# Performance work log

Measured on AMD Instinct MI355X. Metric: run time of the kernel, lower is better.

Reference implementation:

```python
import jax, jax.numpy as jnp
import numpy as np

B, D_IN, H1, D_OUT = 32768, 256, 256, 64
E, T, MU = 32, 16, 0.01


def setup_inputs() -> dict:
    key = jax.random.key(0)
    ks = jax.random.split(key, 9)
    s = lambda *sh: 1.0 / np.sqrt(sh[-2])  # not used; torch default init approximated below
    return {
        "backbone_output": jax.random.normal(ks[0], (B, D_IN), dtype=jnp.float32),
        "task": jax.random.randint(ks[1], (B,), 0, T),
        # expert MLP params, stacked across experts (weights stored [E, in, out])
        "W1": jax.random.normal(ks[2], (E, D_IN, H1), dtype=jnp.float32) * (1.0 / np.sqrt(D_IN)),
        "b1": jnp.zeros((E, H1), dtype=jnp.float32),
        "W2": jax.random.normal(ks[3], (E, H1, D_OUT), dtype=jnp.float32) * (1.0 / np.sqrt(H1)),
        "b2": jnp.zeros((E, D_OUT), dtype=jnp.float32),
        # attention params (torch.randn init)
        "task_queries": jax.random.normal(ks[4], (T, D_OUT), dtype=jnp.float32),
        "key_matricies": jax.random.normal(ks[5], (E, D_OUT, D_OUT), dtype=jnp.float32),
        "value_matricies": jax.random.normal(ks[6], (E, D_OUT, D_OUT), dtype=jnp.float32),
    }


def reference(backbone_output, task, W1, b1, W2, b2, task_queries, key_matricies, value_matricies):
    # all experts run densely on the full batch
    h = jax.nn.relu(jnp.einsum('bi,eih->beh', backbone_output, W1) + b1)      # [B,E,H1]
    expert_outputs = jnp.einsum('beh,eho->beo', h, W2) + b2                   # [B,E,D_OUT]
    # per-expert key/value projections
    expert_keys = jnp.einsum('bei,eij->bej', expert_outputs, key_matricies)    # [B,E,D_OUT]
    expert_values = jnp.einsum('bei,eij->bej', expert_outputs, value_matricies)
    # attention over experts using the per-task query
    q = task_queries[task]                                                     # [B,D_OUT]
    attention_scores = jnp.einsum('bej,bj->be', expert_keys, q)                # [B,E]
    attention_weights = jax.nn.softmax(attention_scores, axis=-1)
    tower_input = jnp.einsum('be,bej->bj', attention_weights, expert_values)   # [B,D_OUT]
    eps = jnp.float32(1e-6)
    reg_loss_term = -(1.0 / E) * MU * jnp.sum(attention_weights + eps)
    return tower_input, reg_loss_term
```

## Files before the change

kernel.cpp:

```cpp
#include <hip/hip_runtime.h>
#include <hip/hip_fp16.h>

#define NTHR 512
#define BM   128
#define NBLK 256
#define NEXP 32

using f16x8 = __attribute__((ext_vector_type(8))) _Float16;
using f16x4 = __attribute__((ext_vector_type(4))) _Float16;
using f32x4 = __attribute__((ext_vector_type(4))) float;
using u32x4 = __attribute__((ext_vector_type(4))) unsigned int;
using u32x2 = __attribute__((ext_vector_type(2))) unsigned int;

static constexpr size_t ESTRIDE_B = 182272;

__device__ __forceinline__ unsigned short f2h(float x){
  _Float16 h = (_Float16)x; return __builtin_bit_cast(unsigned short, h);
}

typedef __attribute__((address_space(3))) void lds_void;
typedef const __attribute__((address_space(1))) void glb_void;
__device__ __forceinline__ void gll16(const void* g, void* l){
  __builtin_amdgcn_global_load_lds((glb_void*)g, (lds_void*)l, 16, 0, 0);
}

#define VMW(N)  asm volatile("s_waitcnt vmcnt(" #N ")" ::: "memory")
#define LGKM0   asm volatile("s_waitcnt lgkmcnt(0)" ::: "memory")
#define SB      __builtin_amdgcn_sched_barrier(0)
#define BARRIER do { SB; __builtin_amdgcn_s_barrier(); SB; } while(0)

__global__ __launch_bounds__(256) void prep_w1frag(const float* __restrict__ W1,
                                                   unsigned short* __restrict__ strm){
  const int e = blockIdx.x >> 3, kc = blockIdx.x & 7;
  const float* se = W1 + (size_t)e*65536 + (size_t)kc*32*256;
  unsigned short* de = strm + (size_t)e*91136 + kc*8192;
  for (int fl = threadIdx.x; fl < 1024; fl += 256){
    const int ct = fl >> 6, l = fl & 63;
    const float* s0 = se + (size_t)((l>>4)*8)*256 + ct*16 + (l&15);
    union { unsigned short s[8]; u32x4 v; } h8;
    #pragma unroll
    for (int j = 0; j < 8; j++) h8.s[j] = f2h(s0[(size_t)j*256]);
    *reinterpret_cast<u32x4*>(&de[fl*8]) = h8.v;
  }
}

__global__ __launch_bounds__(256) void prep_wvp(
    const float* __restrict__ W2, const float* __restrict__ V,
    const float* __restrict__ Km, const float* __restrict__ Q,
    const float* __restrict__ b1, const float* __restrict__ b2,
    unsigned short* __restrict__ strm, float* __restrict__ out)
{
  const int e = blockIdx.x >> 3, oct = blockIdx.x & 7;
  const int t = threadIdx.x;
  __shared__ float lv[64*64];
  __shared__ float ktlT[64*16];
  __shared__ float lw2[32*64];

  for (int i = t; i < 1024; i += 256)
    *reinterpret_cast<float4*>(&lv[i*4]) = *reinterpret_cast<const float4*>(V + (size_t)e*4096 + i*4);
  for (int i = t; i < 512; i += 256)
    *reinterpret_cast<float4*>(&lw2[i*4]) = *reinterpret_cast<const float4*>(W2 + (size_t)e*16384 + (size_t)oct*2048 + i*4);
  #pragma unroll
  for (int pass = 0; pass < 4; pass++){
    const int id = t + pass*256;
    const int tt = id >> 6, i = id & 63;
    const float4* Kr = reinterpret_cast<const float4*>(Km + (size_t)(e*64 + i)*64);
    const float4* qr = reinterpret_cast<const float4*>(Q + tt*64);
    float s = 0.f;
    #pragma unroll
    for (int j = 0; j < 16; j++){ float4 a = Kr[j], b = qr[j]; s += a.x*b.x+a.y*b.y+a.z*b.z+a.w*b.w; }
    ktlT[i*16 + tt] = s;
  }
  __syncthreads();

  const int k2 = oct*32 + (t >> 3);
  const int cb = t & 7;
  const int c0 = cb*12;
  const float* w2r = &lw2[(t>>3)*64];
  const float* gp[3]; int gs[3]; bool gv[3];
  #pragma unroll
  for (int q = 0; q < 3; q++){
    const int cg = c0 + q*4;
    gv[q] = (cg < 80);
    if (cg < 64){ gp[q] = &lv[cg];        gs[q] = 64; }
    else        { gp[q] = &ktlT[cg - 64]; gs[q] = 16; }
  }
  float pv[12];
  #pragma unroll
  for (int n = 0; n < 12; n++) pv[n] = 0.f;
  for (int i = 0; i < 64; i++){
    const float w = w2r[i];
    #pragma unroll
    for (int q = 0; q < 3; q++){
      if (gv[q]){
        const float4 vq = *reinterpret_cast<const float4*>(gp[q] + i*gs[q]);
        pv[q*4+0] += w*vq.x; pv[q*4+1] += w*vq.y; pv[q*4+2] += w*vq.z; pv[q*4+3] += w*vq.w;
      }
    }
  }
  const int wn_ = k2 >> 7, fn = (k2 >> 4) & 7, fnp = fn >> 1, half = fn & 1;
  const int g2 = (k2 >> 2) & 3, jj = k2 & 3;
  unsigned short* fb = strm + (size_t)e*91136 + (wn_ ? 77824 : 65536);
  #pragma unroll
  for (int n = 0; n < 12; n++){
    const int cc = c0 + n;
    if (cc < 64){
      const int ct = cc >> 4, lc = cc & 15, l = g2*16 + lc;
      fb[(fnp*6+ct)*512 + l*8 + half*4 + jj] = f2h(pv[n]);
    } else if (cc < 80){
      const int lc = cc - 64, l = g2*16 + lc;
      const float s = pv[n];
      const unsigned short hi = f2h(s);
      const float rem = s - (float)__builtin_bit_cast(_Float16, hi);
      fb[(fnp*6+4)*512 + l*8 + half*4 + jj] = hi;
      fb[(fnp*6+5)*512 + l*8 + half*4 + jj] = f2h(rem);
    }
  }
  if (oct == 0){
    float* b1d = reinterpret_cast<float*>((char*)strm + (size_t)e*ESTRIDE_B + 180224);
    b1d[t] = b1[e*256 + t];
  }
  if (oct == 1 && t < 80){
    float s = 0.f;
    if (t < 64){ for (int i = 0; i < 64; i++) s += b2[e*64+i]*lv[i*64+t]; }
    else       { for (int i = 0; i < 64; i++) s += b2[e*64+i]*ktlT[i*16 + (t-64)]; }
    float* bd = reinterpret_cast<float*>((char*)strm + (size_t)e*ESTRIDE_B + 181248);
    bd[t] = s;
  }
  if (blockIdx.x == 0 && t == 0) out[2097152] = -10.24032768f;
}

__global__ __launch_bounds__(NTHR, 2) __attribute__((amdgpu_waves_per_eu(2, 2)))
void moe_main(const float* __restrict__ X, const int* __restrict__ task,
              const unsigned short* __restrict__ strm, float* __restrict__ out)
{
  __shared__ unsigned short smem[75776];
  unsigned char* exch = (unsigned char*)smem + 98304;

  const int tid  = threadIdx.x;
  const int lane = tid & 63;
  const int wid  = tid >> 6;
  const int g    = lane >> 4;
  const int c    = lane & 15;
  const int wm   = wid >> 1, wn = wid & 1;
  const int row0 = blockIdx.x * BM;

  auto issue48 = [&](const unsigned short* src, int sloth){
    #pragma unroll
    for (int q = 0; q < 6; q++)
      gll16(src + q*4096 + tid*8, &smem[sloth + q*4096 + tid*8]);
  };
  auto issue32 = [&](const unsigned short* src, int sloth){
    #pragma unroll
    for (int q = 0; q < 4; q++)
      gll16(src + q*4096 + tid*8, &smem[sloth + q*4096 + tid*8]);
  };
  auto issueAux = [&](const unsigned short* es_, int k){
    gll16(es_ + 90112 + lane*8, &smem[73728 + k*1024 + lane*8]);
    gll16(es_ + 90624 + lane*8, &smem[73728 + k*1024 + 512 + lane*8]);
  };

  f16x8 af[2][8];
  #pragma unroll
  for (int fm = 0; fm < 2; fm++){
    const float* xr = X + (size_t)(row0 + wm*32 + fm*16 + c)*256;
    #pragma unroll
    for (int kc = 0; kc < 8; kc++){
      const f32x4 v0 = *reinterpret_cast<const f32x4*>(xr + kc*32 + g*8);
      const f32x4 v1 = *reinterpret_cast<const f32x4*>(xr + kc*32 + g*8 + 4);
      union { unsigned short s[8]; f16x8 h; } h8;
      #pragma unroll
      for (int j = 0; j < 4; j++){ h8.s[j] = f2h(v0[j]); h8.s[4+j] = f2h(v1[j]); }
      af[fm][kc] = h8.h;
    }
  }
  const int4 tq = *reinterpret_cast<const int4*>(&task[row0 + wm*32 + wn*16 + g*4]);
  const int tsk4[4] = {tq.x, tq.y, tq.z, tq.w};

  VMW(0);

  issue48(strm,          0);
  issue48(strm + 24576,  24576);
  issueAux(strm, 0);

  f32x4 oacc[4];
  float m_[4], d_[4];
  #pragma unroll
  for (int j = 0; j < 4; j++){
    m_[j] = -1e30f; d_[j] = 0.f;
    #pragma unroll
    for (int ct = 0; ct < 4; ct++) oacc[ct][j] = 0.f;
  }

#define G1STEP(BASEH, KC) do { \
    f16x8 bfr_[8]; \
    _Pragma("unroll") \
    for (int fnl = 0; fnl < 8; fnl++) \
      bfr_[fnl] = *reinterpret_cast<const f16x8*>(&smem[(BASEH) + (wn*8+fnl)*512 + lane*8]); \
    _Pragma("unroll") \
    for (int fnl = 0; fnl < 8; fnl++){ \
      acc1[fnl][0] = __builtin_amdgcn_mfma_f32_16x16x32_f16(bfr_[fnl], af[0][KC], acc1[fnl][0], 0,0,0); \
      acc1[fnl][1] = __builtin_amdgcn_mfma_f32_16x16x32_f16(bfr_[fnl], af[1][KC], acc1[fnl][1], 0,0,0); \
    } \
  } while(0)

#define MSTEP(FNP) do { \
    u32x4 pr[6]; \
    _Pragma("unroll") \
    for (int i = 0; i < 6; i++) \
      pr[i] = *reinterpret_cast<const u32x4*>(&smem[49152 + wn*12288 + ((FNP)*6+i)*512 + lane*8]); \
    const f32x4 b1a = *reinterpret_cast<const f32x4*>(b1f + wn*128 + (2*(FNP)+0)*16 + g*4); \
    const f32x4 b1b = *reinterpret_cast<const f32x4*>(b1f + wn*128 + (2*(FNP)+1)*16 + g*4); \
    _Pragma("unroll") \
    for (int half = 0; half < 2; half++){ \
      const int fnl = (FNP)*2 + half; \
      const f32x4 bb = half ? b1b : b1a; \
      f16x4 a0, a1; \
      _Pragma("unroll") \
      for (int j = 0; j < 4; j++){ \
        a0[j] = (_Float16)fmaxf(acc1[fnl][0][j] + bb[j], 0.f); \
        a1[j] = (_Float16)fmaxf(acc1[fnl][1][j] + bb[j], 0.f); \
      } \
      _Pragma("unroll") \
      for (int ct = 0; ct < 6; ct++){ \
        union { u32x4 v; struct { f16x4 lo, hi; } h; } u; u.v = pr[ct]; \
        const f16x4 bfr = half ? u.h.hi : u.h.lo; \
        const int ci = (ct < 5) ? ct : 4; \
        p0[ci] = __builtin_amdgcn_mfma_f32_16x16x16f16(a0, bfr, p0[ci], 0,0,0); \
        p1[ci] = __builtin_amdgcn_mfma_f32_16x16x16f16(a1, bfr, p1[ci], 0,0,0); \
      } \
    } \
  } while(0)

#define XW(ACC, EB) do { \
    _Pragma("unroll") \
    for (int ct = 0; ct < 4; ct++){ \
      union { unsigned short s[4]; u32x2 v; } p_; \
      _Pragma("unroll") \
      for (int j = 0; j < 4; j++) p_.s[j] = f2h(ACC[ct][j]); \
      *reinterpret_cast<u32x2*>((EB) + ct*512 + lane*8) = p_.v; \
    } \
    *reinterpret_cast<f32x4*>((EB) + 2048 + lane*16) = ACC[4]; \
  } while(0)

#define XFIN(B2F) do { \
    const unsigned char* ebS = exch + (wm*2 + wn)*6144 + wn*3072; \
    const unsigned char* ebP = exch + (wm*2 + (wn^1))*6144 + wn*3072; \
    float b2c[4]; \
    _Pragma("unroll") \
    for (int ct = 0; ct < 4; ct++) b2c[ct] = (B2F)[ct*16 + c]; \
    const float b2s = (B2F)[64 + c]; \
    f32x4 pvv[4]; \
    _Pragma("unroll") \
    for (int ct = 0; ct < 4; ct++){ \
      union { u32x2 v; unsigned short s[4]; } pa_, pb_; \
      pa_.v = *reinterpret_cast<const u32x2*>(ebS + ct*512 + lane*8); \
      pb_.v = *reinterpret_cast<const u32x2*>(ebP + ct*512 + lane*8); \
      _Pragma("unroll") \
      for (int j = 0; j < 4; j++) \
        pvv[ct][j] = (float)__builtin_bit_cast(_Float16, pa_.s[j]) \
                   + (float)__builtin_bit_cast(_Float16, pb_.s[j]) + b2c[ct]; \
    } \
    const f32x4 s1 = *reinterpret_cast<const f32x4*>(ebS + 2048 + lane*16); \
    const f32x4 s2 = *reinterpret_cast<const f32x4*>(ebP + 2048 + lane*16); \
    _Pragma("unroll") \
    for (int j = 0; j < 4; j++){ \
      const float sv = s1[j] + s2[j] + b2s; \
      const float s  = __shfl(sv, (lane & 48) | tsk4[j]); \
      const float mn = fmaxf(m_[j], s); \
      const float al = __expf(m_[j] - mn); \
      const float p  = __expf(s - mn); \
      d_[j] = d_[j]*al + p; \
      m_[j] = mn; \
      _Pragma("unroll") \
      for (int ct = 0; ct < 4; ct++) \
        oacc[ct][j] = oacc[ct][j]*al + p*pvv[ct][j]; \
    } \
  } while(0)

  for (int e = 0; e < NEXP; e++){
    const unsigned short* es  = strm + (size_t)e*91136;
    const unsigned short* esn = (e == NEXP-1) ? strm : es + 91136;
    const int pA = (e & 1) * 24576;
    const int pB = 24576 - pA;
    const float* b1f = reinterpret_cast<const float*>(&smem[73728 + (e & 1)*1024]);
    f32x4 acc1[8][2] = {};

    VMW(8); BARRIER;
    G1STEP(pA,          0);
    if (e > 0){
      const float* b2p = reinterpret_cast<const float*>(&smem[73728 + ((e+1) & 1)*1024]) + 256;
      XFIN(b2p);
    }
    G1STEP(pA +  8192,  1);
    G1STEP(pA + 16384,  2);

    VMW(2); BARRIER;
    issue32(es + 49152, pA);
    issue48(es + 65536, 49152);
    G1STEP(pB,          3);
    G1STEP(pB +  8192,  4);
    G1STEP(pB + 16384,  5);

    VMW(6); BARRIER;
    issue48(esn, pB);
    G1STEP(pA,          6);
    G1STEP(pA +  8192,  7);

    VMW(6); BARRIER;
    issue48(esn + 24576, pA);
    f32x4 p0[5] = {}, p1[5] = {};
    MSTEP(0); MSTEP(1); MSTEP(2); MSTEP(3);

    BARRIER;
    {
      unsigned char* eb = exch + wid*6144;
      XW(p0, eb);
      XW(p1, eb + 3072);
    }
    issueAux(esn, (e+1) & 1);
    LGKM0;
  }

  BARRIER;
  {
    const float* b2p = reinterpret_cast<const float*>(&smem[73728 + (31 & 1)*1024]) + 256;
    XFIN(b2p);
  }
#undef XFIN
#undef XW
#undef MSTEP
#undef G1STEP

  #pragma unroll
  for (int j = 0; j < 4; j++){
    const float inv = 1.f / d_[j];
    float* orow = out + (size_t)(row0 + wm*32 + wn*16 + g*4 + j)*64;
    #pragma unroll
    for (int ct = 0; ct < 4; ct++)
      orow[ct*16 + c] = oacc[ct][j]*inv;
  }
}

extern "C" void kernel_launch(void* const* d_in, const int* in_sizes, int n_in,
                              void* d_out, int out_size, void* d_ws, size_t ws_size,
                              hipStream_t hs)
{
  (void)in_sizes; (void)n_in; (void)out_size; (void)ws_size;
  const float* X   = (const float*)d_in[0];
  const int*   tsk = (const int*)  d_in[1];
  const float* W1  = (const float*)d_in[2];
  const float* b1  = (const float*)d_in[3];
  const float* W2  = (const float*)d_in[4];
  const float* b2  = (const float*)d_in[5];
  const float* Q   = (const float*)d_in[6];
  const float* Km  = (const float*)d_in[7];
  const float* Vm  = (const float*)d_in[8];
  float* out = (float*)d_out;

  unsigned short* strm = (unsigned short*)d_ws;

  prep_w1frag<<<dim3(256), dim3(256), 0, hs>>>(W1, strm);
  prep_wvp  <<<dim3(256), dim3(256), 0, hs>>>(W2, Vm, Km, Q, b1, b2, strm, out);
  moe_main  <<<dim3(NBLK), dim3(NTHR), 0, hs>>>(X, tsk, strm, out);
}
```

Measured before the change: 242.9 us.

## Halve block to 4 waves, stage X in LDS, stream W1 in small double-buffered chunks

The main kernel moves from 8 waves to 4 waves per block. Each wave now computes 64 rows instead of 32, so it keeps 8x4 MFMA accumulators. The fp16-converted X tile is stored in shared memory and A fragments are reloaded per K-step, replacing the register-resident copy. W1 is streamed in 16 KB chunks through two LDS slots, with one barrier per K-step, and the second-GEMM partial exchange between wave pairs is reorganised to match. The aim is to raise MFMA work per B-fragment load and change the latency and occupancy balance. The cost is more LDS reads for A, more barriers, higher register pressure, and fewer waves available to hide latency.

```diff
diff --git a/kernel.cpp b/kernel.cpp
--- a/kernel.cpp
+++ b/kernel.cpp
@@ -1,7 +1,7 @@
 #include <hip/hip_runtime.h>
 #include <hip/hip_fp16.h>
 
-#define NTHR 512
+#define NTHR 256
 #define BM   128
 #define NBLK 256
 #define NEXP 32
@@ -130,7 +130,7 @@
   if (blockIdx.x == 0 && t == 0) out[2097152] = -10.24032768f;
 }
 
-__global__ __launch_bounds__(NTHR, 2) __attribute__((amdgpu_waves_per_eu(2, 2)))
+__global__ __launch_bounds__(NTHR, 1)
 void moe_main(const float* __restrict__ X, const int* __restrict__ task,
               const unsigned short* __restrict__ strm, float* __restrict__ out)
 {
@@ -145,63 +145,73 @@
   const int wm   = wid >> 1, wn = wid & 1;
   const int row0 = blockIdx.x * BM;
 
-  auto issue48 = [&](const unsigned short* src, int sloth){
+  auto issue16 = [&](const unsigned short* src, int sloth){
+    #pragma unroll
+    for (int q = 0; q < 4; q++)
+      gll16(src + q*2048 + tid*8, &smem[sloth + q*2048 + tid*8]);
+  };
+  auto issueM = [&](const unsigned short* es_, int half){
     #pragma unroll
     for (int q = 0; q < 6; q++)
-      gll16(src + q*4096 + tid*8, &smem[sloth + q*4096 + tid*8]);
-  };
-  auto issue32 = [&](const unsigned short* src, int sloth){
-    #pragma unroll
-    for (int q = 0; q < 4; q++)
-      gll16(src + q*4096 + tid*8, &smem[sloth + q*4096 + tid*8]);
+      gll16(es_ + 65536 + half*12288 + q*2048 + tid*8,
+            &smem[49152 + half*12288 + q*2048 + tid*8]);
   };
   auto issueAux = [&](const unsigned short* es_, int k){
     gll16(es_ + 90112 + lane*8, &smem[73728 + k*1024 + lane*8]);
     gll16(es_ + 90624 + lane*8, &smem[73728 + k*1024 + 512 + lane*8]);
   };
 
-  f16x8 af[2][8];
-  #pragma unroll
-  for (int fm = 0; fm < 2; fm++){
-    const float* xr = X + (size_t)(row0 + wm*32 + fm*16 + c)*256;
-    #pragma unroll
-    for (int kc = 0; kc < 8; kc++){
-      const f32x4 v0 = *reinterpret_cast<const f32x4*>(xr + kc*32 + g*8);
-      const f32x4 v1 = *reinterpret_cast<const f32x4*>(xr + kc*32 + g*8 + 4);
-      union { unsigned short s[8]; f16x8 h; } h8;
+  #pragma unroll
+  for (int p = 0; p < 16; p++){
+    const int id  = p*256 + tid;
+    const int row = id >> 5, k0 = (id & 31)*8;
+    const float4 v0 = *reinterpret_cast<const float4*>(X + (size_t)(row0+row)*256 + k0);
+    const float4 v1 = *reinterpret_cast<const float4*>(X + (size_t)(row0+row)*256 + k0 + 4);
+    union { unsigned short s[8]; u32x4 v; } h8;
+    h8.s[0]=f2h(v0.x); h8.s[1]=f2h(v0.y); h8.s[2]=f2h(v0.z); h8.s[3]=f2h(v0.w);
+    h8.s[4]=f2h(v1.x); h8.s[5]=f2h(v1.y); h8.s[6]=f2h(v1.z); h8.s[7]=f2h(v1.w);
+    const int l = (row & 15) | (((k0 >> 3) & 3) << 4);
+    *reinterpret_cast<u32x4*>(&smem[((row>>4)*8 + (k0>>5))*512 + l*8]) = h8.v;
+  }
+
+  int tsk[2][4];
+  {
+    const int4 qa = *reinterpret_cast<const int4*>(&task[row0 + wm*64 + (wn*2+0)*16 + g*4]);
+    const int4 qb = *reinterpret_cast<const int4*>(&task[row0 + wm*64 + (wn*2+1)*16 + g*4]);
+    tsk[0][0]=qa.x; tsk[0][1]=qa.y; tsk[0][2]=qa.z; tsk[0][3]=qa.w;
+    tsk[1][0]=qb.x; tsk[1][1]=qb.y; tsk[1][2]=qb.z; tsk[1][3]=qb.w;
+  }
+
+  issueAux(strm, 0);
+  issue16(strm,         32768);
+  issue16(strm +  8192, 40960);
+  LGKM0;
+
+  f32x4 oacc[2][4];
+  float m_[2][4], d_[2][4];
+  #pragma unroll
+  for (int o = 0; o < 2; o++)
+    #pragma unroll
+    for (int j = 0; j < 4; j++){
+      m_[o][j] = -1e30f; d_[o][j] = 0.f;
       #pragma unroll
-      for (int j = 0; j < 4; j++){ h8.s[j] = f2h(v0[j]); h8.s[4+j] = f2h(v1[j]); }
-      af[fm][kc] = h8.h;
-    }
-  }
-  const int4 tq = *reinterpret_cast<const int4*>(&task[row0 + wm*32 + wn*16 + g*4]);
-  const int tsk4[4] = {tq.x, tq.y, tq.z, tq.w};
-
-  VMW(0);
-
-  issue48(strm,          0);
-  issue48(strm + 24576,  24576);
-  issueAux(strm, 0);
-
-  f32x4 oacc[4];
-  float m_[4], d_[4];
-  #pragma unroll
-  for (int j = 0; j < 4; j++){
-    m_[j] = -1e30f; d_[j] = 0.f;
-    #pragma unroll
-    for (int ct = 0; ct < 4; ct++) oacc[ct][j] = 0.f;
-  }
-
-#define G1STEP(BASEH, KC) do { \
-    f16x8 bfr_[8]; \
+      for (int ct = 0; ct < 4; ct++) oacc[o][ct][j] = 0.f;
+    }
+  f32x4 p[4][5];
+
+#define G1STEP(SLOTH, KC) do { \
+    f16x8 bf_[8], ab_[4]; \
     _Pragma("unroll") \
     for (int fnl = 0; fnl < 8; fnl++) \
-      bfr_[fnl] = *reinterpret_cast<const f16x8*>(&smem[(BASEH) + (wn*8+fnl)*512 + lane*8]); \
-    _Pragma("unroll") \
-    for (int fnl = 0; fnl < 8; fnl++){ \
-      acc1[fnl][0] = __builtin_amdgcn_mfma_f32_16x16x32_f16(bfr_[fnl], af[0][KC], acc1[fnl][0], 0,0,0); \
-      acc1[fnl][1] = __builtin_amdgcn_mfma_f32_16x16x32_f16(bfr_[fnl], af[1][KC], acc1[fnl][1], 0,0,0); \
-    } \
+      bf_[fnl] = *reinterpret_cast<const f16x8*>(&smem[(SLOTH) + (wn*8+fnl)*512 + lane*8]); \
+    _Pragma("unroll") \
+    for (int fmi = 0; fmi < 4; fmi++) \
+      ab_[fmi] = *reinterpret_cast<const f16x8*>(&smem[((wm*4+fmi)*8 + (KC))*512 + lane*8]); \
+    _Pragma("unroll") \
+    for (int fnl = 0; fnl < 8; fnl++) \
+      _Pragma("unroll") \
+      for (int fmi = 0; fmi < 4; fmi++) \
+        acc1[fnl][fmi] = __builtin_amdgcn_mfma_f32_16x16x32_f16(bf_[fnl], ab_[fmi], acc1[fnl][fmi], 0,0,0); \
   } while(0)
 
 #define MSTEP(FNP) do { \
@@ -215,130 +225,128 @@
     for (int half = 0; half < 2; half++){ \
       const int fnl = (FNP)*2 + half; \
       const f32x4 bb = half ? b1b : b1a; \
-      f16x4 a0, a1; \
+      f16x4 a0, a1, a2, a3; \
       _Pragma("unroll") \
       for (int j = 0; j < 4; j++){ \
         a0[j] = (_Float16)fmaxf(acc1[fnl][0][j] + bb[j], 0.f); \
         a1[j] = (_Float16)fmaxf(acc1[fnl][1][j] + bb[j], 0.f); \
+        a2[j] = (_Float16)fmaxf(acc1[fnl][2][j] + bb[j], 0.f); \
+        a3[j] = (_Float16)fmaxf(acc1[fnl][3][j] + bb[j], 0.f); \
       } \
       _Pragma("unroll") \
       for (int ct = 0; ct < 6; ct++){ \
         union { u32x4 v; struct { f16x4 lo, hi; } h; } u; u.v = pr[ct]; \
         const f16x4 bfr = half ? u.h.hi : u.h.lo; \
         const int ci = (ct < 5) ? ct : 4; \
-        p0[ci] = __builtin_amdgcn_mfma_f32_16x16x16f16(a0, bfr, p0[ci], 0,0,0); \
-        p1[ci] = __builtin_amdgcn_mfma_f32_16x16x16f16(a1, bfr, p1[ci], 0,0,0); \
+        p[0][ci] = __builtin_amdgcn_mfma_f32_16x16x16f16(a0, bfr, p[0][ci], 0,0,0); \
+        p[1][ci] = __builtin_amdgcn_mfma_f32_16x16x16f16(a1, bfr, p[1][ci], 0,0,0); \
+        p[2][ci] = __builtin_amdgcn_mfma_f32_16x16x16f16(a2, bfr, p[2][ci], 0,0,0); \
+        p[3][ci] = __builtin_amdgcn_mfma_f32_16x16x16f16(a3, bfr, p[3][ci], 0,0,0); \
       } \
-    } \
-  } while(0)
-
-#define XW(ACC, EB) do { \
+    } } while(0)
+
+#define XW1(ACC, SLOT) do { \
+    unsigned char* eb_ = exch + (SLOT)*3072; \
     _Pragma("unroll") \
     for (int ct = 0; ct < 4; ct++){ \
       union { unsigned short s[4]; u32x2 v; } p_; \
       _Pragma("unroll") \
       for (int j = 0; j < 4; j++) p_.s[j] = f2h(ACC[ct][j]); \
-      *reinterpret_cast<u32x2*>((EB) + ct*512 + lane*8) = p_.v; \
+      *reinterpret_cast<u32x2*>(eb_ + ct*512 + lane*8) = p_.v; \
     } \
-    *reinterpret_cast<f32x4*>((EB) + 2048 + lane*16) = ACC[4]; \
+    *reinterpret_cast<f32x4*>(eb_ + 2048 + lane*16) = ACC[4]; \
   } while(0)
 
-#define XFIN(B2F) do { \
-    const unsigned char* ebS = exch + (wm*2 + wn)*6144 + wn*3072; \
-    const unsigned char* ebP = exch + (wm*2 + (wn^1))*6144 + wn*3072; \
+#define XFIN1(ACC, SLOT, OI) do { \
+    const unsigned char* eb_ = exch + (SLOT)*3072; \
+    f32x4 pvv[4]; \
+    _Pragma("unroll") \
+    for (int ct = 0; ct < 4; ct++){ \
+      union { u32x2 v; unsigned short s[4]; } pb_; \
+      pb_.v = *reinterpret_cast<const u32x2*>(eb_ + ct*512 + lane*8); \
+      _Pragma("unroll") \
+      for (int j = 0; j < 4; j++) \
+        pvv[ct][j] = ACC[ct][j] + (float)__builtin_bit_cast(_Float16, pb_.s[j]) + b2c[ct]; \
+    } \
+    const f32x4 s2 = *reinterpret_cast<const f32x4*>(eb_ + 2048 + lane*16); \
+    _Pragma("unroll") \
+    for (int j = 0; j < 4; j++){ \
+      const float sv = ACC[4][j] + s2[j] + b2s; \
+      const float s  = __shfl(sv, (lane & 48) | tsk[OI][j]); \
+      const float mn = fmaxf(m_[OI][j], s); \
+      const float al = __expf(m_[OI][j] - mn); \
+      const float pe = __expf(s - mn); \
+      d_[OI][j] = d_[OI][j]*al + pe; \
+      m_[OI][j] = mn; \
+      _Pragma("unroll") \
+      for (int ct = 0; ct < 4; ct++) \
+        oacc[OI][ct][j] = oacc[OI][ct][j]*al + pe*pvv[ct][j]; \
+    } } while(0)
+
+#define XFINALL(B2F) do { \
     float b2c[4]; \
     _Pragma("unroll") \
     for (int ct = 0; ct < 4; ct++) b2c[ct] = (B2F)[ct*16 + c]; \
     const float b2s = (B2F)[64 + c]; \
-    f32x4 pvv[4]; \
-    _Pragma("unroll") \
-    for (int ct = 0; ct < 4; ct++){ \
-      union { u32x2 v; unsigned short s[4]; } pa_, pb_; \
-      pa_.v = *reinterpret_cast<const u32x2*>(ebS + ct*512 + lane*8); \
-      pb_.v = *reinterpret_cast<const u32x2*>(ebP + ct*512 + lane*8); \
-      _Pragma("unroll") \
-      for (int j = 0; j < 4; j++) \
-        pvv[ct][j] = (float)__builtin_bit_cast(_Float16, pa_.s[j]) \
-                   + (float)__builtin_bit_cast(_Float16, pb_.s[j]) + b2c[ct]; \
-    } \
-    const f32x4 s1 = *reinterpret_cast<const f32x4*>(ebS + 2048 + lane*16); \
-    const f32x4 s2 = *reinterpret_cast<const f32x4*>(ebP + 2048 + lane*16); \
-    _Pragma("unroll") \
-    for (int j = 0; j < 4; j++){ \
-      const float sv = s1[j] + s2[j] + b2s; \
-      const float s  = __shfl(sv, (lane & 48) | tsk4[j]); \
-      const float mn = fmaxf(m_[j], s); \
-      const float al = __expf(m_[j] - mn); \
-      const float p  = __expf(s - mn); \
-      d_[j] = d_[j]*al + p; \
-      m_[j] = mn; \
-      _Pragma("unroll") \
-      for (int ct = 0; ct < 4; ct++) \
-        oacc[ct][j] = oacc[ct][j]*al + p*pvv[ct][j]; \
-    } \
+    if (wn == 0){ XFIN1(p[0], wm*4+0, 0); XFIN1(p[1], wm*4+1, 1); } \
+    else        { XFIN1(p[2], wm*4+2, 0); XFIN1(p[3], wm*4+3, 1); } \
   } while(0)
 
   for (int e = 0; e < NEXP; e++){
     const unsigned short* es  = strm + (size_t)e*91136;
     const unsigned short* esn = (e == NEXP-1) ? strm : es + 91136;
-    const int pA = (e & 1) * 24576;
-    const int pB = 24576 - pA;
     const float* b1f = reinterpret_cast<const float*>(&smem[73728 + (e & 1)*1024]);
-    f32x4 acc1[8][2] = {};
-
-    VMW(8); BARRIER;
-    G1STEP(pA,          0);
+    f32x4 acc1[8][4] = {};
+
+    VMW(4); BARRIER;
+    G1STEP(32768, 0);
     if (e > 0){
       const float* b2p = reinterpret_cast<const float*>(&smem[73728 + ((e+1) & 1)*1024]) + 256;
-      XFIN(b2p);
-    }
-    G1STEP(pA +  8192,  1);
-    G1STEP(pA + 16384,  2);
-
-    VMW(2); BARRIER;
-    issue32(es + 49152, pA);
-    issue48(es + 65536, 49152);
-    G1STEP(pB,          3);
-    G1STEP(pB +  8192,  4);
-    G1STEP(pB + 16384,  5);
+      XFINALL(b2p);
+    }
+    VMW(0); BARRIER; issue16(es + 2*8192, 32768);                    G1STEP(40960, 1);
+    VMW(0); BARRIER; issue16(es + 3*8192, 40960);                    G1STEP(32768, 2);
+    VMW(0); BARRIER; issue16(es + 4*8192, 32768);                    G1STEP(40960, 3);
+    VMW(0); BARRIER; issue16(es + 5*8192, 40960); issueM(es, 0);     G1STEP(32768, 4);
+    VMW(6); BARRIER; issue16(es + 6*8192, 32768); issueM(es, 1);     G1STEP(40960, 5);
+    VMW(6); BARRIER; issue16(es + 7*8192, 40960); issueAux(esn, (e+1)&1); G1STEP(32768, 6);
+    VMW(2); BARRIER; issue16(esn,         32768);                    G1STEP(40960, 7);
 
     VMW(6); BARRIER;
-    issue48(esn, pB);
-    G1STEP(pA,          6);
-    G1STEP(pA +  8192,  7);
-
-    VMW(6); BARRIER;
-    issue48(esn + 24576, pA);
-    f32x4 p0[5] = {}, p1[5] = {};
+    issue16(esn + 8192, 40960);
+    #pragma unroll
+    for (int f = 0; f < 4; f++)
+      #pragma unroll
+      for (int ci = 0; ci < 5; ci++) p[f][ci] = (f32x4){0.f,0.f,0.f,0.f};
     MSTEP(0); MSTEP(1); MSTEP(2); MSTEP(3);
 
     BARRIER;
-    {
-      unsigned char* eb = exch + wid*6144;
-      XW(p0, eb);
-      XW(p1, eb + 3072);
-    }
-    issueAux(esn, (e+1) & 1);
+    if (wn == 0){ XW1(p[2], wm*4+2); XW1(p[3], wm*4+3); }
+    else        { XW1(p[0], wm*4+0); XW1(p[1], wm*4+1); }
     LGKM0;
   }
 
   BARRIER;
   {
-    const float* b2p = reinterpret_cast<const float*>(&smem[73728 + (31 & 1)*1024]) + 256;
-    XFIN(b2p);
-  }
-#undef XFIN
-#undef XW
+    const float* b2p = reinterpret_cast<const float*>(&smem[73728 + 1*1024]) + 256;
+    XFINALL(b2p);
+  }
+#undef XFINALL
+#undef XFIN1
+#undef XW1
 #undef MSTEP
 #undef G1STEP
 
   #pragma unroll
-  for (int j = 0; j < 4; j++){
-    const float inv = 1.f / d_[j];
-    float* orow = out + (size_t)(row0 + wm*32 + wn*16 + g*4 + j)*64;
-    #pragma unroll
-    for (int ct = 0; ct < 4; ct++)
-      orow[ct*16 + c] = oacc[ct][j]*inv;
+  for (int fmo = 0; fmo < 2; fmo++){
+    #pragma unroll
+    for (int j = 0; j < 4; j++){
+      const float inv = 1.f / d_[fmo][j];
+      float* orow = out + (size_t)(row0 + wm*64 + (wn*2+fmo)*16 + g*4 + j)*64;
+      #pragma unroll
+      for (int ct = 0; ct < 4; ct++)
+        orow[ct*16 + c] = oacc[fmo][ct][j]*inv;
+    }
   }
 }
 
```

After: 291.3 us. +19.9%, slower.
